# Performance work log

Hardware: AMD Instinct MI355X
Metric: run time of the kernel (lower is better)

Reference implementation:

```python
import jax, jax.numpy as jnp
import numpy as np
import math

NUM_HEADS = 32
NUM_KV_HEADS = 8
HEAD_DIM = 64
ROPE_THETA = 150000.0


def rotate_half(x):
    half = x.shape[-1] // 2
    return jnp.concatenate([-x[..., half:], x[..., :half]], axis=-1)


def setup_inputs() -> dict:
    key = jax.random.key(0)
    k1, k2, k3, k4, k5 = jax.random.split(key, 5)
    B, S, H = 2, 2048, 2048
    qkv_size = (NUM_HEADS + 2 * NUM_KV_HEADS) * HEAD_DIM  # 3072
    scale = 1.0 / math.sqrt(H)
    return {
        "hidden_states": jax.random.normal(k1, (B, S, H), jnp.float32),
        "position_ids": jnp.arange(S, dtype=jnp.int64 if jax.config.jax_enable_x64 else jnp.int32)[None, :],
        "qkv_w": jax.random.normal(k2, (qkv_size, H), jnp.float32) * scale,
        "qkv_b": jax.random.normal(k3, (qkv_size,), jnp.float32) * 0.01,
        "o_w": jax.random.normal(k4, (H, NUM_HEADS * HEAD_DIM), jnp.float32) * scale,
        "o_b": jax.random.normal(k5, (H,), jnp.float32) * 0.01,
    }


def reference(hidden_states, position_ids, qkv_w, qkv_b, o_w, o_b):
    B, S, _ = hidden_states.shape
    g = NUM_HEADS // NUM_KV_HEADS  # query heads per kv head
    d = HEAD_DIM

    qkv = hidden_states @ qkv_w.T + qkv_b  # [B,S,(H+2KV)*d]
    qkv = qkv.reshape(B, S, NUM_KV_HEADS, g + 2, d)
    q = qkv[:, :, :, :g, :].reshape(B, S, NUM_HEADS, d).transpose(0, 2, 1, 3)   # [B,Hq,S,d]
    k = qkv[:, :, :, g, :].transpose(0, 2, 1, 3)                                 # [B,Hkv,S,d]
    v = qkv[:, :, :, g + 1, :].transpose(0, 2, 1, 3)                             # [B,Hkv,S,d]

    # HF-style RoPE: cos/sin [S, d]
    inv_freq = 1.0 / (ROPE_THETA ** (jnp.arange(0, d, 2, dtype=jnp.float32) / d))
    freqs = jnp.outer(position_ids.reshape(-1).astype(jnp.float32), inv_freq)    # [S, d/2]
    emb = jnp.concatenate([freqs, freqs], axis=-1)                               # [S, d]
    cos = jnp.cos(emb)[None, None]                                               # [1,1,S,d]
    sin = jnp.sin(emb)[None, None]
    q = q * cos + rotate_half(q) * sin
    k = k * cos + rotate_half(k) * sin

    # GQA: repeat_interleave kv heads to match query heads
    k = jnp.repeat(k, g, axis=1)  # [B,Hq,S,d]
    v = jnp.repeat(v, g, axis=1)

    scores = jnp.einsum("bhqd,bhkd->bhqk", q, k) / math.sqrt(d)  # [B,Hq,S,S]
    attn = jax.nn.softmax(scores, axis=-1)
    out = jnp.einsum("bhqk,bhkd->bhqd", attn, v)
    out = out.transpose(0, 2, 1, 3).reshape(B, S, NUM_HEADS * d)
    return out @ o_w.T + o_b
```

## Files before the change

### kernel.cpp

```cpp
#include <hip/hip_runtime.h>
#include <math.h>

#define NHQ 32
#define NKV 8
#define HD 64
#define QKV_DIM 3072
#define MODEL_DIM 2048
#define QSCALE 0.1803368801111204f

typedef __attribute__((ext_vector_type(4))) float     f32x4;
typedef __attribute__((ext_vector_type(8))) _Float16  half8;
typedef __attribute__((ext_vector_type(4))) _Float16  half4v;
typedef __attribute__((ext_vector_type(2))) __fp16    fp16x2;

#define ASYNC_COPY16(g, l)                                                        \
    __builtin_amdgcn_global_load_lds(                                             \
        (const __attribute__((address_space(1))) void*)(g),                       \
        (__attribute__((address_space(3))) void*)(l), 16, 0, 0)

__device__ __forceinline__ float fast_exp2(float x)
{
#if __has_builtin(__builtin_amdgcn_exp2f)
    return __builtin_amdgcn_exp2f(x);
#else
    float r;
    asm volatile("v_exp_f32 %0, %1\ns_nop 0" : "=v"(r) : "v"(x));
    return r;
#endif
}

__global__ __launch_bounds__(256)
void f32_to_f16_kernel(const float* __restrict__ src, _Float16* __restrict__ dst, int n4)
{
    int i = blockIdx.x * 256 + threadIdx.x;
    if (i < n4) {
        float4 v = ((const float4*)src)[i];
        half4v h = { (_Float16)v.x, (_Float16)v.y, (_Float16)v.z, (_Float16)v.w };
        ((half4v*)dst)[i] = h;
    }
}

__global__ __launch_bounds__(256)
void sincos_table_kernel(const int* __restrict__ pos, float* __restrict__ tab, int S)
{
    int i = blockIdx.x * 256 + threadIdx.x;
    if (i < S * 32) {
        int s = i >> 5, fi = i & 31;
        float p = (float)pos[s];
        float inv_freq = powf(150000.0f, -(float)fi * (1.0f / 32.0f));
        float ang = p * inv_freq;
        tab[s * 64 + fi]      = cosf(ang);
        tab[s * 64 + 32 + fi] = sinf(ang);
    }
}

template<int MODE>
__global__ __launch_bounds__(256)
void gemm_f16_mfma(const _Float16* __restrict__ A, const _Float16* __restrict__ W,
                   const float* __restrict__ bias, void* __restrict__ Cout,
                   const float* __restrict__ tab, int M, int N, int K, int S)
{
    __shared__ _Float16 As[128 * 32];
    __shared__ _Float16 Bs[128 * 32];

    const int t    = threadIdx.x;
    const int w    = t >> 6;
    const int lane = t & 63;
    const int quad = lane >> 4, l15 = lane & 15;
    const size_t m0 = (size_t)blockIdx.y * 128;
    const size_t n0 = (size_t)blockIdx.x * 128;
    const int wm = (w >> 1) * 64, wn = (w & 1) * 64;

    const int row0 = t >> 2;
    const int sub  = (t & 3) * 8;
    const _Float16* ag0 = A + (m0 + row0) * K + sub;
    const _Float16* ag1 = A + (m0 + 64 + row0) * K + sub;
    const _Float16* bg0 = W + (n0 + row0) * K + sub;
    const _Float16* bg1 = W + (n0 + 64 + row0) * K + sub;
    _Float16* al0 = &As[w * 512];
    _Float16* al1 = &As[2048 + w * 512];
    _Float16* bl0 = &Bs[w * 512];
    _Float16* bl1 = &Bs[2048 + w * 512];

    f32x4 acc[4][4];
#pragma unroll
    for (int i = 0; i < 4; i++)
#pragma unroll
        for (int j = 0; j < 4; j++) acc[i][j] = (f32x4){0.f, 0.f, 0.f, 0.f};

    for (int k0 = 0; k0 < K; k0 += 32) {
        ASYNC_COPY16(ag0 + k0, al0);
        ASYNC_COPY16(ag1 + k0, al1);
        ASYNC_COPY16(bg0 + k0, bl0);
        ASYNC_COPY16(bg1 + k0, bl1);
        __syncthreads();

        half8 af[4], bf[4];
#pragma unroll
        for (int i = 0; i < 4; i++) {
            af[i] = *(const half8*)&As[(wm + i * 16 + l15) * 32 + quad * 8];
            bf[i] = *(const half8*)&Bs[(wn + i * 16 + l15) * 32 + quad * 8];
        }
#pragma unroll
        for (int i = 0; i < 4; i++)
#pragma unroll
            for (int j = 0; j < 4; j++)
                acc[i][j] = __builtin_amdgcn_mfma_f32_16x16x32_f16(af[i], bf[j], acc[i][j], 0, 0, 0);
        __syncthreads();
    }

    float bv[4];
#pragma unroll
    for (int j = 0; j < 4; j++) bv[j] = bias[n0 + wn + j * 16 + l15];

    const int ct = (int)(((n0 + wn) >> 6) % 6);

#pragma unroll
    for (int i = 0; i < 4; i++)
#pragma unroll
        for (int r = 0; r < 4; r++) {
            const size_t row = m0 + wm + i * 16 + quad * 4 + r;
            float v[4];
#pragma unroll
            for (int j = 0; j < 4; j++) v[j] = acc[i][j][r] + bv[j];

            if (MODE == 2 && ct != 5) {
                const float* tc = tab + (size_t)(row % S) * 64;
                const float ca = tc[l15],      sa = tc[32 + l15];
                const float cb = tc[16 + l15], sb = tc[48 + l15];
                const float qs = (ct < 4) ? QSCALE : 1.0f;
                const float n0v = v[0] * ca - v[2] * sa;
                const float n1v = v[1] * cb - v[3] * sb;
                const float n2v = v[2] * ca + v[0] * sa;
                const float n3v = v[3] * cb + v[1] * sb;
                v[0] = n0v * qs; v[1] = n1v * qs; v[2] = n2v * qs; v[3] = n3v * qs;
            }

            const size_t col = n0 + wn + l15;
#pragma unroll
            for (int j = 0; j < 4; j++) {
                if (MODE != 0) ((_Float16*)Cout)[row * N + col + j * 16] = (_Float16)v[j];
                else           ((float*)Cout)[row * N + col + j * 16] = v[j];
            }
        }
}

__global__ __launch_bounds__(256)
void transpose_v_kernel(const _Float16* __restrict__ qkv, _Float16* __restrict__ vtg, int BS)
{
    __shared__ _Float16 tile[64 * 72];
    const int t = threadIdx.x;
    const int tb = blockIdx.x * 64;
    const int g = blockIdx.y;
    const int voff = (g * 6 + 5) * 64;

    const int tok = t >> 2, dsub = (t & 3) * 16;
    const _Float16* src = qkv + (size_t)(tb + tok) * QKV_DIM + voff + dsub;
    *(half8*)&tile[tok * 72 + dsub]     = *(const half8*)(src);
    *(half8*)&tile[tok * 72 + dsub + 8] = *(const half8*)(src + 8);
    __syncthreads();

    const int d = t >> 2, tsub = (t & 3) * 16;
    half8 a, c;
#pragma unroll
    for (int i = 0; i < 8; i++) a[i] = tile[(tsub + i) * 72 + d];
#pragma unroll
    for (int i = 0; i < 8; i++) c[i] = tile[(tsub + 8 + i) * 72 + d];
    _Float16* dst = vtg + ((size_t)g * 64 + d) * BS + tb + tsub;
    *(half8*)dst       = a;
    *(half8*)(dst + 8) = c;
}

__global__ __launch_bounds__(256)
void attn_mfma(const _Float16* __restrict__ qkv, const _Float16* __restrict__ vtg,
               _Float16* __restrict__ out, int B, int S)
{
    __shared__ _Float16 Ks[64 * 72];
    __shared__ _Float16 VsT[80 * 72];
    __shared__ _Float16 Ps[4][32 * 72];

    const int t = threadIdx.x, w = t >> 6, lane = t & 63;
    const int quad = lane >> 4, l15 = lane & 15;
    const int b = blockIdx.z, g = blockIdx.y;
    const int q0 = blockIdx.x * 32;
    const int qoff = (g * 6 + w) * 64;
    const int koff = (g * 6 + 4) * 64;

    half8 qf[2][2];
#pragma unroll
    for (int s = 0; s < 2; s++) {
        const _Float16* qp = qkv + (size_t)(b * S + q0 + s * 16 + l15) * QKV_DIM + qoff;
        qf[s][0] = *(const half8*)(qp + quad * 8);
        qf[s][1] = *(const half8*)(qp + 32 + quad * 8);
    }

    for (int idx = 64 * 72 + t; idx < 80 * 72; idx += 256)
        VsT[idx] = (idx < 65 * 72) ? (_Float16)1.0f : (_Float16)0.0f;

    f32x4 O[2][4], L[2];
#pragma unroll
    for (int s = 0; s < 2; s++) {
        L[s] = (f32x4){0.f, 0.f, 0.f, 0.f};
#pragma unroll
        for (int dt = 0; dt < 4; dt++) O[s][dt] = (f32x4){0.f, 0.f, 0.f, 0.f};
    }

    const int kst_tok = t >> 2;
    const int kst_d   = (t & 3) * 16;
    const int vst_d   = t >> 3;
    const int vst_sub = (t & 7) * 8;

    const _Float16* kbase  = qkv + (size_t)(b * S + kst_tok) * QKV_DIM + koff + kst_d;
    const _Float16* vbase0 = vtg + ((size_t)g * 64 + vst_d) * (size_t)(B * S) + b * S + vst_sub;
    const _Float16* vbase1 = vtg + ((size_t)g * 64 + 32 + vst_d) * (size_t)(B * S) + b * S + vst_sub;

    half8 kr0 = *(const half8*)(kbase);
    half8 kr1 = *(const half8*)(kbase + 8);
    half8 vr0 = *(const half8*)(vbase0);
    half8 vr1 = *(const half8*)(vbase1);

    for (int kt = 0; kt < S; kt += 64) {
        *(half8*)&Ks[kst_tok * 72 + kst_d]      = kr0;
        *(half8*)&Ks[kst_tok * 72 + kst_d + 8]  = kr1;
        *(half8*)&VsT[vst_d * 72 + vst_sub]        = vr0;
        *(half8*)&VsT[(32 + vst_d) * 72 + vst_sub] = vr1;
        __syncthreads();

        if (kt + 64 < S) {
            kr0 = *(const half8*)(kbase + (size_t)(kt + 64) * QKV_DIM);
            kr1 = *(const half8*)(kbase + (size_t)(kt + 64) * QKV_DIM + 8);
            vr0 = *(const half8*)(vbase0 + kt + 64);
            vr1 = *(const half8*)(vbase1 + kt + 64);
        }

        half8 kf[4][2];
#pragma unroll
        for (int mt = 0; mt < 4; mt++) {
            kf[mt][0] = *(const half8*)&Ks[(mt * 16 + l15) * 72 + quad * 8];
            kf[mt][1] = *(const half8*)&Ks[(mt * 16 + l15) * 72 + 32 + quad * 8];
        }
        f32x4 sacc[2][4];
#pragma unroll
        for (int s = 0; s < 2; s++)
#pragma unroll
            for (int mt = 0; mt < 4; mt++) {
                f32x4 z = (f32x4){0.f, 0.f, 0.f, 0.f};
                z = __builtin_amdgcn_mfma_f32_16x16x32_f16(kf[mt][0], qf[s][0], z, 0, 0, 0);
                z = __builtin_amdgcn_mfma_f32_16x16x32_f16(kf[mt][1], qf[s][1], z, 0, 0, 0);
                sacc[s][mt] = z;
            }

#pragma unroll
        for (int s = 0; s < 2; s++)
#pragma unroll
            for (int mt = 0; mt < 4; mt++) {
                fp16x2 pa = __builtin_amdgcn_cvt_pkrtz(fast_exp2(sacc[s][mt][0]),
                                                       fast_exp2(sacc[s][mt][1]));
                fp16x2 pb = __builtin_amdgcn_cvt_pkrtz(fast_exp2(sacc[s][mt][2]),
                                                       fast_exp2(sacc[s][mt][3]));
                uint2 u;
                u.x = __builtin_bit_cast(unsigned int, pa);
                u.y = __builtin_bit_cast(unsigned int, pb);
                *(uint2*)&Ps[w][(s * 16 + l15) * 72 + mt * 16 + quad * 4] = u;
            }
        asm volatile("s_waitcnt lgkmcnt(0)" ::: "memory");

        half8 pf[2][2];
#pragma unroll
        for (int s = 0; s < 2; s++) {
            pf[s][0] = *(const half8*)&Ps[w][(s * 16 + l15) * 72 + quad * 8];
            pf[s][1] = *(const half8*)&Ps[w][(s * 16 + l15) * 72 + 32 + quad * 8];
        }
#pragma unroll
        for (int dt = 0; dt < 4; dt++) {
            half8 vv0 = *(const half8*)&VsT[(dt * 16 + l15) * 72 + quad * 8];
            half8 vv1 = *(const half8*)&VsT[(dt * 16 + l15) * 72 + 32 + quad * 8];
#pragma unroll
            for (int s = 0; s < 2; s++) {
                O[s][dt] = __builtin_amdgcn_mfma_f32_16x16x32_f16(pf[s][0], vv0, O[s][dt], 0, 0, 0);
                O[s][dt] = __builtin_amdgcn_mfma_f32_16x16x32_f16(pf[s][1], vv1, O[s][dt], 0, 0, 0);
            }
        }
        {
            half8 lv0 = *(const half8*)&VsT[(64 + l15) * 72 + quad * 8];
            half8 lv1 = *(const half8*)&VsT[(64 + l15) * 72 + 32 + quad * 8];
#pragma unroll
            for (int s = 0; s < 2; s++) {
                L[s] = __builtin_amdgcn_mfma_f32_16x16x32_f16(pf[s][0], lv0, L[s], 0, 0, 0);
                L[s] = __builtin_amdgcn_mfma_f32_16x16x32_f16(pf[s][1], lv1, L[s], 0, 0, 0);
            }
        }
        __syncthreads();
    }

    const int hq = g * 4 + w;
#pragma unroll
    for (int s = 0; s < 2; s++)
#pragma unroll
        for (int r = 0; r < 4; r++) {
            const float lr = __shfl(L[s][r], lane & 48, 64);
            const float ir = 1.0f / lr;
            const size_t row = (size_t)(b * S + q0 + s * 16 + quad * 4 + r);
#pragma unroll
            for (int dt = 0; dt < 4; dt++)
                out[row * (NHQ * HD) + hq * 64 + dt * 16 + l15] = (_Float16)(O[s][dt][r] * ir);
        }
}

extern "C" void kernel_launch(void* const* d_in, const int* in_sizes, int n_in,
                              void* d_out, int out_size, void* d_ws, size_t ws_size,
                              hipStream_t stream)
{
    const float* hidden = (const float*)d_in[0];
    const int*   pos    = (const int*)d_in[1];
    const float* qkv_w  = (const float*)d_in[2];
    const float* qkv_b  = (const float*)d_in[3];
    const float* o_w    = (const float*)d_in[4];
    const float* o_b    = (const float*)d_in[5];
    float* out = (float*)d_out;

    const int S  = in_sizes[1];
    const int BS = in_sizes[0] / MODEL_DIM;
    const int B  = BS / S;

    _Float16* hA   = (_Float16*)d_ws;
    _Float16* hW1  = hA   + (size_t)BS * MODEL_DIM;
    _Float16* hW2  = hW1  + (size_t)QKV_DIM * MODEL_DIM;
    _Float16* qkvh = hW2  + (size_t)MODEL_DIM * MODEL_DIM;
    _Float16* atth = qkvh + (size_t)BS * QKV_DIM;
    float*    tab  = (float*)(atth + (size_t)BS * MODEL_DIM);
    _Float16* vtg  = (_Float16*)(tab + (size_t)S * 64);

    f32_to_f16_kernel<<<(BS * MODEL_DIM / 4 + 255) / 256, 256, 0, stream>>>(hidden, hA, BS * MODEL_DIM / 4);
    f32_to_f16_kernel<<<(QKV_DIM * MODEL_DIM / 4 + 255) / 256, 256, 0, stream>>>(qkv_w, hW1, QKV_DIM * MODEL_DIM / 4);
    f32_to_f16_kernel<<<(MODEL_DIM * MODEL_DIM / 4 + 255) / 256, 256, 0, stream>>>(o_w, hW2, MODEL_DIM * MODEL_DIM / 4);
    sincos_table_kernel<<<(S * 32 + 255) / 256, 256, 0, stream>>>(pos, tab, S);

    gemm_f16_mfma<2><<<dim3(QKV_DIM / 128, BS / 128), 256, 0, stream>>>(
        hA, hW1, qkv_b, qkvh, tab, BS, QKV_DIM, MODEL_DIM, S);

    transpose_v_kernel<<<dim3(BS / 64, NKV), 256, 0, stream>>>(qkvh, vtg, BS);

    attn_mfma<<<dim3(S / 32, NKV, B), 256, 0, stream>>>(qkvh, vtg, atth, B, S);

    gemm_f16_mfma<0><<<dim3(MODEL_DIM / 128, BS / 128), 256, 0, stream>>>(
        atth, hW2, o_b, out, nullptr, BS, MODEL_DIM, MODEL_DIM, S);
}
```

Measured before the change: 369.4 us.

## Triple-buffer GEMM LDS tiles with async prefetch and XOR swizzle

```diff
diff --git a/kernel.cpp b/kernel.cpp
--- a/kernel.cpp
+++ b/kernel.cpp
@@ -55,13 +55,13 @@
 }
 
 template<int MODE>
-__global__ __launch_bounds__(256)
+__global__ __launch_bounds__(256, 3)
 void gemm_f16_mfma(const _Float16* __restrict__ A, const _Float16* __restrict__ W,
                    const float* __restrict__ bias, void* __restrict__ Cout,
                    const float* __restrict__ tab, int M, int N, int K, int S)
 {
-    __shared__ _Float16 As[128 * 32];
-    __shared__ _Float16 Bs[128 * 32];
+    __shared__ _Float16 As[3][128 * 32];
+    __shared__ _Float16 Bs[3][128 * 32];
 
     const int t    = threadIdx.x;
     const int w    = t >> 6;
@@ -71,16 +71,14 @@
     const size_t n0 = (size_t)blockIdx.x * 128;
     const int wm = (w >> 1) * 64, wn = (w & 1) * 64;
 
-    const int row0 = t >> 2;
-    const int sub  = (t & 3) * 8;
-    const _Float16* ag0 = A + (m0 + row0) * K + sub;
-    const _Float16* ag1 = A + (m0 + 64 + row0) * K + sub;
-    const _Float16* bg0 = W + (n0 + row0) * K + sub;
-    const _Float16* bg1 = W + (n0 + 64 + row0) * K + sub;
-    _Float16* al0 = &As[w * 512];
-    _Float16* al1 = &As[2048 + w * 512];
-    _Float16* bl0 = &Bs[w * 512];
-    _Float16* bl1 = &Bs[2048 + w * 512];
+    const int sr   = t >> 2;
+    const int klog = ((t & 3) ^ ((sr >> 1) & 3)) * 8;
+    const _Float16* ag0 = A + (m0 + sr) * K + klog;
+    const _Float16* ag1 = A + (m0 + 64 + sr) * K + klog;
+    const _Float16* bg0 = W + (n0 + sr) * K + klog;
+    const _Float16* bg1 = W + (n0 + 64 + sr) * K + klog;
+
+    const int xk8 = (quad ^ ((l15 >> 1) & 3)) * 8;
 
     f32x4 acc[4][4];
 #pragma unroll
@@ -88,26 +86,57 @@
 #pragma unroll
         for (int j = 0; j < 4; j++) acc[i][j] = (f32x4){0.f, 0.f, 0.f, 0.f};
 
-    for (int k0 = 0; k0 < K; k0 += 32) {
-        ASYNC_COPY16(ag0 + k0, al0);
-        ASYNC_COPY16(ag1 + k0, al1);
-        ASYNC_COPY16(bg0 + k0, bl0);
-        ASYNC_COPY16(bg1 + k0, bl1);
-        __syncthreads();
+    const int nt = K >> 5;
+
+#define STAGE_TILE(bi, kt_)                                         \
+    do {                                                            \
+        const int _k0 = (kt_) * 32;                                 \
+        ASYNC_COPY16(ag0 + _k0, &As[bi][w * 512]);                  \
+        ASYNC_COPY16(ag1 + _k0, &As[bi][2048 + w * 512]);           \
+        ASYNC_COPY16(bg0 + _k0, &Bs[bi][w * 512]);                  \
+        ASYNC_COPY16(bg1 + _k0, &Bs[bi][2048 + w * 512]);           \
+    } while (0)
+
+    STAGE_TILE(0, 0);
+    STAGE_TILE(1, 1);
+    asm volatile("s_waitcnt vmcnt(4)" ::: "memory");
+    __builtin_amdgcn_s_barrier();
+    __builtin_amdgcn_sched_barrier(0);
+
+    int bc = 0;
+    for (int kt = 0; kt < nt; ++kt) {
+        const _Float16* Ab = &As[bc][0];
+        const _Float16* Bb = &Bs[bc][0];
 
         half8 af[4], bf[4];
 #pragma unroll
         for (int i = 0; i < 4; i++) {
-            af[i] = *(const half8*)&As[(wm + i * 16 + l15) * 32 + quad * 8];
-            bf[i] = *(const half8*)&Bs[(wn + i * 16 + l15) * 32 + quad * 8];
-        }
+            af[i] = *(const half8*)(Ab + (wm + i * 16 + l15) * 32 + xk8);
+            bf[i] = *(const half8*)(Bb + (wn + i * 16 + l15) * 32 + xk8);
+        }
+
+        if (kt + 2 < nt) {
+            int bs = bc + 2; if (bs >= 3) bs -= 3;
+            STAGE_TILE(bs, kt + 2);
+        }
+
+        __builtin_amdgcn_s_setprio(1);
 #pragma unroll
         for (int i = 0; i < 4; i++)
 #pragma unroll
             for (int j = 0; j < 4; j++)
                 acc[i][j] = __builtin_amdgcn_mfma_f32_16x16x32_f16(af[i], bf[j], acc[i][j], 0, 0, 0);
-        __syncthreads();
-    }
+        __builtin_amdgcn_s_setprio(0);
+
+        if (kt + 1 < nt) {
+            if (kt + 2 < nt) asm volatile("s_waitcnt vmcnt(4)" ::: "memory");
+            else             asm volatile("s_waitcnt vmcnt(0)" ::: "memory");
+            __builtin_amdgcn_s_barrier();
+            __builtin_amdgcn_sched_barrier(0);
+        }
+        bc = bc + 1; if (bc == 3) bc = 0;
+    }
+#undef STAGE_TILE
 
     float bv[4];
 #pragma unroll
```

Measured after the change: 331.4 us. 1.11x faster.
